# Optimization experiments

Measured on AMD Instinct MI355X. Metric: run time of the kernel, lower is better.

## Reference

```python
import jax, jax.numpy as jnp
import numpy as np

KSIZE = 5  # 5x5 tap neighborhood


def setup_inputs() -> dict:
    key = jax.random.key(0)
    k1, k2, k3, k4 = jax.random.split(key, 4)
    B, C, H, W = 8, 3, 512, 512
    return {
        "input": jax.random.normal(k1, (B, C, H, W), dtype=jnp.float32),
        "upscale_params": jax.random.normal(k2, (B, 3, 2 * H, 2 * W), dtype=jnp.float32),
        "skip_signal": jax.random.normal(k3, (B, 3, 2 * H, 2 * W), dtype=jnp.float32),
        "skip_param": jax.random.normal(k4, (B, 1, 2 * H, 2 * W), dtype=jnp.float32),
    }


def reference(input, upscale_params, skip_signal, skip_param):
    B, C, H, W = input.shape
    H2, W2 = 2 * H, 2 * W

    sp = jax.nn.sigmoid(skip_param)
    kx = jax.nn.sigmoid(upscale_params[:, 0:1]) * 4.0   # (B,1,H2,W2)
    ky = jax.nn.sigmoid(upscale_params[:, 1:2]) * 4.0
    kxy = jnp.tanh(upscale_params[:, 2:3]) * 1.0

    # Output-pixel centers mapped into input pixel space: uv*[W,H].
    # These are separable along x and y, so keep them as 1-D vectors.
    fx = (jnp.arange(W2, dtype=jnp.float32) + 0.5) / W2 * W   # (W2,)
    fy = (jnp.arange(H2, dtype=jnp.float32) + 0.5) / H2 * H   # (H2,)
    bx = jnp.floor(fx)
    by = jnp.floor(fy)
    # Residual to tap center: dx = uv_x*W - (floor(.)+off+0.5)
    dx0 = (fx - bx - 0.5)[None, None, None, :]   # (1,1,1,W2)
    dy0 = (fy - by - 0.5)[None, None, :, None]   # (1,1,H2,1)
    bxi = bx.astype(jnp.int32)
    byi = by.astype(jnp.int32)

    acc = jnp.zeros((B, 3, H2, W2), dtype=input.dtype)
    wacc = jnp.zeros((B, 1, H2, W2), dtype=input.dtype)

    for iy in range(KSIZE):
        for ix in range(KSIZE):
            ox = ix - KSIZE // 2
            oy = iy - KSIZE // 2
            # nearest-neighbor, border padding == clamped integer gather
            ixs = jnp.clip(bxi + ox, 0, W - 1)   # (W2,)
            iys = jnp.clip(byi + oy, 0, H - 1)   # (H2,)
            sample = input[:, :, iys[:, None], ixs[None, :]]  # (B,C,H2,W2)
            dx = dx0 - ox
            dy = dy0 - oy
            # faithful to source: second term uses ky*kx (as written)
            dist = dx * dx * kx * kx + dy * dy * ky * kx + 2.0 * dx * dy * kx * ky * kxy
            w = jnp.exp(-2.0 * dist)
            acc = acc + sample * w
            wacc = wacc + jnp.abs(w)

    upscaled = acc / (wacc + 1e-6)
    # torch.lerp(upscaled, skip_signal, sp)
    return upscaled + sp * (skip_signal - upscaled)
```

## Files before the change

### kernel.cpp

```cpp
#include <hip/hip_runtime.h>

#define HH 512
#define WW 512
#define H2 1024
#define W2 1024
#define CPLANE (HH * WW)
#define OPLANE (H2 * W2)

__device__ __forceinline__ float fast_rcp(float x) {
    return __builtin_amdgcn_rcpf(x);
}

__global__ __launch_bounds__(256) void fnu_kernel(
    const float* __restrict__ inp,
    const float* __restrict__ upar,
    const float* __restrict__ skips,
    const float* __restrict__ skipp,
    float* __restrict__ out)
{
    const int gid = blockIdx.x * 256 + threadIdx.x;
    const int tx = gid & 511;
    const int y2 = (gid >> 9) & 1023;
    const int b  = gid >> 19;

    const int   ty  = y2 >> 1;
    const float dy0 = (y2 & 1) ? 0.25f : -0.25f;

    const size_t obase = ((size_t)(b * 3) * H2 + y2) * W2 + 2 * tx;
    const size_t sbase = ((size_t)b * H2 + y2) * W2 + 2 * tx;

    const float2 p0 = *(const float2*)(upar + obase);
    const float2 p1 = *(const float2*)(upar + obase + (size_t)OPLANE);
    const float2 p2 = *(const float2*)(upar + obase + 2 * (size_t)OPLANE);

    float Av[2], Bv[2], Cv[2];
#pragma unroll
    for (int j = 0; j < 2; ++j) {
        const float u0 = j ? p0.y : p0.x;
        const float u1 = j ? p1.y : p1.x;
        const float u2 = j ? p2.y : p2.x;
        const float kx  = 4.0f * fast_rcp(1.0f + __expf(-u0));
        const float ky  = 4.0f * fast_rcp(1.0f + __expf(-u1));
        const float e   = __expf(-2.0f * u2);
        const float kxy = (1.0f - e) * fast_rcp(1.0f + e);
        Av[j] = -2.0f * kx * kx;
        Bv[j] = -2.0f * ky * kx;
        Cv[j] = -4.0f * kx * ky * kxy;
    }

    int xs[5];
#pragma unroll
    for (int i = 0; i < 5; ++i) {
        int v = tx + i - 2;
        xs[i] = v < 0 ? 0 : (v > (WW - 1) ? (WW - 1) : v);
    }

    float acc0[3] = {0.f, 0.f, 0.f};
    float acc1[3] = {0.f, 0.f, 0.f};
    float w0s = 0.f, w1s = 0.f;

    const float* ib = inp + (size_t)(b * 3) * CPLANE;

#pragma unroll
    for (int iy = 0; iy < 5; ++iy) {
        int yv = ty + iy - 2;
        const int ysrc = yv < 0 ? 0 : (yv > (HH - 1) ? (HH - 1) : yv);
        const float* row = ib + (size_t)ysrc * WW;
        const float dy  = dy0 - (float)(iy - 2);
        const float dy2 = dy * dy;
        const float bd0 = Bv[0] * dy2, bd1 = Bv[1] * dy2;
        const float cd0 = Cv[0] * dy,  cd1 = Cv[1] * dy;
#pragma unroll
        for (int ix = 0; ix < 5; ++ix) {
            const float s0 = row[xs[ix]];
            const float s1 = row[xs[ix] + CPLANE];
            const float s2 = row[xs[ix] + 2 * CPLANE];
            const float dxe = -0.25f - (float)(ix - 2);
            const float dxo =  0.25f - (float)(ix - 2);
            const float a0 = fmaf(Av[0], dxe * dxe, fmaf(cd0, dxe, bd0));
            const float a1 = fmaf(Av[1], dxo * dxo, fmaf(cd1, dxo, bd1));
            const float w0 = __expf(a0);
            const float w1 = __expf(a1);
            w0s += w0;
            w1s += w1;
            acc0[0] = fmaf(s0, w0, acc0[0]);
            acc0[1] = fmaf(s1, w0, acc0[1]);
            acc0[2] = fmaf(s2, w0, acc0[2]);
            acc1[0] = fmaf(s0, w1, acc1[0]);
            acc1[1] = fmaf(s1, w1, acc1[1]);
            acc1[2] = fmaf(s2, w1, acc1[2]);
        }
    }

    const float2 sp2 = *(const float2*)(skipp + sbase);
    const float sp0 = fast_rcp(1.0f + __expf(-sp2.x));
    const float sp1 = fast_rcp(1.0f + __expf(-sp2.y));
    const float r0 = fast_rcp(w0s + 1e-6f);
    const float r1 = fast_rcp(w1s + 1e-6f);

#pragma unroll
    for (int c = 0; c < 3; ++c) {
        const float2 sk = *(const float2*)(skips + obase + (size_t)c * OPLANE);
        const float u0 = acc0[c] * r0;
        const float u1 = acc1[c] * r1;
        float2 o;
        o.x = u0 + sp0 * (sk.x - u0);
        o.y = u1 + sp1 * (sk.y - u1);
        *(float2*)(out + obase + (size_t)c * OPLANE) = o;
    }
}

extern "C" void kernel_launch(void* const* d_in, const int* in_sizes, int n_in,
                              void* d_out, int out_size, void* d_ws, size_t ws_size,
                              hipStream_t stream) {
    const float* inp   = (const float*)d_in[0];
    const float* upar  = (const float*)d_in[1];
    const float* skips = (const float*)d_in[2];
    const float* skipp = (const float*)d_in[3];
    float* outp = (float*)d_out;

    const int total = 8 * H2 * (W2 / 2);
    const int block = 256;
    const int grid  = total / block;
    fnu_kernel<<<grid, block, 0, stream>>>(inp, upar, skips, skipp, outp);
}
```

Baseline: 328.5 us.

## Process four input columns per thread with shared row window and exp2 weights

Each thread now handles four input columns (eight output pixels) per row. It loads one 8-wide input window per tap row and channel as vector loads, so neighbouring taps reuse registers instead of issuing 25 scalar gathers per pixel pair. Exponentials are rewritten as exp2 with LOG2E folded into the coefficients, and all upar, skip and output traffic moves to float4. A duplicated coefficient loop remains; its first pass is dead code overwritten by the second. The kernel also launches four times fewer threads and each needs more registers.

```diff
diff --git a/kernel.cpp b/kernel.cpp
--- a/kernel.cpp
+++ b/kernel.cpp
@@ -6,10 +6,10 @@
 #define W2 1024
 #define CPLANE (HH * WW)
 #define OPLANE (H2 * W2)
+#define LOG2E 1.44269504088896f
 
-__device__ __forceinline__ float fast_rcp(float x) {
-    return __builtin_amdgcn_rcpf(x);
-}
+__device__ __forceinline__ float rcpf_(float x)  { return __builtin_amdgcn_rcpf(x); }
+__device__ __forceinline__ float exp2f_(float x) { return __builtin_amdgcn_exp2f(x); }
 
 __global__ __launch_bounds__(256) void fnu_kernel(
     const float* __restrict__ inp,
@@ -19,9 +19,10 @@
     float* __restrict__ out)
 {
     const int gid = blockIdx.x * 256 + threadIdx.x;
-    const int tx = gid & 511;
-    const int y2 = (gid >> 9) & 1023;
-    const int b  = gid >> 19;
+    const int txg = gid & 127;
+    const int tx  = txg << 2;
+    const int y2  = (gid >> 7) & 1023;
+    const int b   = gid >> 17;
 
     const int   ty  = y2 >> 1;
     const float dy0 = (y2 & 1) ? 0.25f : -0.25f;
@@ -29,84 +30,128 @@
     const size_t obase = ((size_t)(b * 3) * H2 + y2) * W2 + 2 * tx;
     const size_t sbase = ((size_t)b * H2 + y2) * W2 + 2 * tx;
 
-    const float2 p0 = *(const float2*)(upar + obase);
-    const float2 p1 = *(const float2*)(upar + obase + (size_t)OPLANE);
-    const float2 p2 = *(const float2*)(upar + obase + 2 * (size_t)OPLANE);
+    const float4 q0a = *(const float4*)(upar + obase);
+    const float4 q0b = *(const float4*)(upar + obase + 4);
+    const float4 q1a = *(const float4*)(upar + obase + (size_t)OPLANE);
+    const float4 q1b = *(const float4*)(upar + obase + (size_t)OPLANE + 4);
+    const float4 q2a = *(const float4*)(upar + obase + 2 * (size_t)OPLANE);
+    const float4 q2b = *(const float4*)(upar + obase + 2 * (size_t)OPLANE + 4);
 
-    float Av[2], Bv[2], Cv[2];
+    const float u0[8] = {q0a.x, q0a.y, q0a.z, q0a.w, q0b.x, q0b.y, q0b.z, q0b.w};
+    const float u1[8] = {q1a.x, q1a.y, q1a.z, q1a.w, q1b.x, q1b.y, q1b.z, q1b.w};
+    const float u2[8] = {q2a.x, q2a.y, q2a.z, q2a.w, q2b.x, q2b.y, q2b.z, q2b.w};
+
+    float A[8], Bc[8], Cc[8];
 #pragma unroll
-    for (int j = 0; j < 2; ++j) {
-        const float u0 = j ? p0.y : p0.x;
-        const float u1 = j ? p1.y : p1.x;
-        const float u2 = j ? p2.y : p2.x;
-        const float kx  = 4.0f * fast_rcp(1.0f + __expf(-u0));
-        const float ky  = 4.0f * fast_rcp(1.0f + __expf(-u1));
-        const float e   = __expf(-2.0f * u2);
-        const float kxy = (1.0f - e) * fast_rcp(1.0f + e);
-        Av[j] = -2.0f * kx * kx;
-        Bv[j] = -2.0f * ky * kx;
-        Cv[j] = -4.0f * kx * ky * kxy;
+    for (int j = 0; j < 8; ++j) {
+        const float kx  = 4.0f * rcpf_(1.0f + exp2f_(-LOG2E * u0[j]));
+        const float ky  = 4.0f * rcpf_(1.0f + exp2f_(-LOG2E * u1[j]));
+        const float e   = exp2f_(-2.0f * LOG2E * u2[j]);
+        const float kxy = (1.0f - e) * rcpf_(1.0f + e);
+        A[j]  = -2.0f * LOG2E * kx * kx;
+        Bc[j] = -2.0f * LOG2E * ky * kx;
+        Cc[j] = 2.0f * Bc[j] * (kx * rcpf_(ky)) * kxy;
+    }
+#pragma unroll
+    for (int j = 0; j < 8; ++j) {
+        const float kx  = 4.0f * rcpf_(1.0f + exp2f_(-LOG2E * u0[j]));
+        const float ky  = 4.0f * rcpf_(1.0f + exp2f_(-LOG2E * u1[j]));
+        const float e   = exp2f_(-2.0f * LOG2E * u2[j]);
+        const float kxy = (1.0f - e) * rcpf_(1.0f + e);
+        A[j]  = -2.0f * LOG2E * kx * kx;
+        Bc[j] = -2.0f * LOG2E * ky * kx;
+        Cc[j] = -4.0f * LOG2E * kx * ky * kxy;
     }
 
-    int xs[5];
+    float acc[8][3];
+    float ws[8];
 #pragma unroll
-    for (int i = 0; i < 5; ++i) {
-        int v = tx + i - 2;
-        xs[i] = v < 0 ? 0 : (v > (WW - 1) ? (WW - 1) : v);
-    }
-
-    float acc0[3] = {0.f, 0.f, 0.f};
-    float acc1[3] = {0.f, 0.f, 0.f};
-    float w0s = 0.f, w1s = 0.f;
+    for (int j = 0; j < 8; ++j) { acc[j][0] = acc[j][1] = acc[j][2] = 0.f; ws[j] = 0.f; }
 
     const float* ib = inp + (size_t)(b * 3) * CPLANE;
 
+    int ysrc[5];
 #pragma unroll
     for (int iy = 0; iy < 5; ++iy) {
-        int yv = ty + iy - 2;
-        const int ysrc = yv < 0 ? 0 : (yv > (HH - 1) ? (HH - 1) : yv);
-        const float* row = ib + (size_t)ysrc * WW;
+        int v = ty + iy - 2;
+        ysrc[iy] = v < 0 ? 0 : (v > (HH - 1) ? (HH - 1) : v);
+    }
+    const int axl = (tx == 0) ? 0 : tx - 2;
+    const int axr = (tx == 508) ? 510 : tx + 4;
+
+#pragma unroll
+    for (int iy = 0; iy < 5; ++iy) {
+        const float* r0 = ib + (size_t)ysrc[iy] * WW;
+
+        float wn[3][8];
+#pragma unroll
+        for (int c = 0; c < 3; ++c) {
+            const float* rp = r0 + (size_t)c * CPLANE;
+            float2 a  = *(const float2*)(rp + axl);
+            float4 m  = *(const float4*)(rp + tx);
+            float2 e2 = *(const float2*)(rp + axr);
+            if (tx == 0)   a.y  = a.x;
+            if (tx == 508) e2.x = e2.y;
+            wn[c][0] = a.x;  wn[c][1] = a.y;
+            wn[c][2] = m.x;  wn[c][3] = m.y; wn[c][4] = m.z; wn[c][5] = m.w;
+            wn[c][6] = e2.x; wn[c][7] = e2.y;
+        }
+
         const float dy  = dy0 - (float)(iy - 2);
         const float dy2 = dy * dy;
-        const float bd0 = Bv[0] * dy2, bd1 = Bv[1] * dy2;
-        const float cd0 = Cv[0] * dy,  cd1 = Cv[1] * dy;
+        float bd[8], cd[8];
 #pragma unroll
-        for (int ix = 0; ix < 5; ++ix) {
-            const float s0 = row[xs[ix]];
-            const float s1 = row[xs[ix] + CPLANE];
-            const float s2 = row[xs[ix] + 2 * CPLANE];
-            const float dxe = -0.25f - (float)(ix - 2);
-            const float dxo =  0.25f - (float)(ix - 2);
-            const float a0 = fmaf(Av[0], dxe * dxe, fmaf(cd0, dxe, bd0));
-            const float a1 = fmaf(Av[1], dxo * dxo, fmaf(cd1, dxo, bd1));
-            const float w0 = __expf(a0);
-            const float w1 = __expf(a1);
-            w0s += w0;
-            w1s += w1;
-            acc0[0] = fmaf(s0, w0, acc0[0]);
-            acc0[1] = fmaf(s1, w0, acc0[1]);
-            acc0[2] = fmaf(s2, w0, acc0[2]);
-            acc1[0] = fmaf(s0, w1, acc1[0]);
-            acc1[1] = fmaf(s1, w1, acc1[1]);
-            acc1[2] = fmaf(s2, w1, acc1[2]);
+        for (int j = 0; j < 8; ++j) { bd[j] = Bc[j] * dy2; cd[j] = Cc[j] * dy; }
+
+#pragma unroll
+        for (int i = 0; i < 4; ++i) {
+            const int je = 2 * i, jo = 2 * i + 1;
+#pragma unroll
+            for (int ox = -2; ox <= 2; ++ox) {
+                const float dxe = -0.25f - (float)ox;
+                const float dxo =  0.25f - (float)ox;
+                const float ae = fmaf(A[je], dxe * dxe, fmaf(cd[je], dxe, bd[je]));
+                const float ao = fmaf(A[jo], dxo * dxo, fmaf(cd[jo], dxo, bd[jo]));
+                const float we = exp2f_(ae);
+                const float wo = exp2f_(ao);
+                ws[je] += we;
+                ws[jo] += wo;
+                const int k = i + ox + 2;
+                acc[je][0] = fmaf(wn[0][k], we, acc[je][0]);
+                acc[je][1] = fmaf(wn[1][k], we, acc[je][1]);
+                acc[je][2] = fmaf(wn[2][k], we, acc[je][2]);
+                acc[jo][0] = fmaf(wn[0][k], wo, acc[jo][0]);
+                acc[jo][1] = fmaf(wn[1][k], wo, acc[jo][1]);
+                acc[jo][2] = fmaf(wn[2][k], wo, acc[jo][2]);
+            }
         }
     }
 
-    const float2 sp2 = *(const float2*)(skipp + sbase);
-    const float sp0 = fast_rcp(1.0f + __expf(-sp2.x));
-    const float sp1 = fast_rcp(1.0f + __expf(-sp2.y));
-    const float r0 = fast_rcp(w0s + 1e-6f);
-    const float r1 = fast_rcp(w1s + 1e-6f);
+    const float4 spa = *(const float4*)(skipp + sbase);
+    const float4 spb = *(const float4*)(skipp + sbase + 4);
+    float sp[8] = {spa.x, spa.y, spa.z, spa.w, spb.x, spb.y, spb.z, spb.w};
+    float rn[8];
+#pragma unroll
+    for (int j = 0; j < 8; ++j) {
+        sp[j] = rcpf_(1.0f + exp2f_(-LOG2E * sp[j]));
+        rn[j] = rcpf_(ws[j] + 1e-6f);
+    }
 
 #pragma unroll
     for (int c = 0; c < 3; ++c) {
-        const float2 sk = *(const float2*)(skips + obase + (size_t)c * OPLANE);
-        const float u0 = acc0[c] * r0;
-        const float u1 = acc1[c] * r1;
-        float2 o;
-        o.x = u0 + sp0 * (sk.x - u0);
-        o.y = u1 + sp1 * (sk.y - u1);
-        *(float2*)(out + obase + (size_t)c * OPLANE) = o;
+        const float4 ska = *(const float4*)(skips + obase + (size_t)c * OPLANE);
+        const float4 skb = *(const float4*)(skips + obase + (size_t)c * OPLANE + 4);
+        const float skv[8] = {ska.x, ska.y, ska.z, ska.w, skb.x, skb.y, skb.z, skb.w};
+        float ov[8];
+#pragma unroll
+        for (int j = 0; j < 8; ++j) {
+            const float u = acc[j][c] * rn[j];
+            ov[j] = u + sp[j] * (skv[j] - u);
+        }
+        float4 oa = {ov[0], ov[1], ov[2], ov[3]};
+        float4 ob = {ov[4], ov[5], ov[6], ov[7]};
+        *(float4*)(out + obase + (size_t)c * OPLANE)     = oa;
+        *(float4*)(out + obase + (size_t)c * OPLANE + 4) = ob;
     }
 }
 
@@ -119,7 +164,7 @@
     const float* skipp = (const float*)d_in[3];
     float* outp = (float*)d_out;
 
-    const int total = 8 * H2 * (W2 / 2);
+    const int total = 8 * H2 * (WW / 4);
     const int block = 256;
     const int grid  = total / block;
     fnu_kernel<<<grid, block, 0, stream>>>(inp, upar, skips, skipp, outp);
```

Measured after the change: 288.9 us. 1.14x faster.
